# Optimization experiments

Hardware: AMD Instinct MI355X
Metric: run time of the kernel (lower is better)

Reference implementation:

```python
import jax, jax.numpy as jnp
import numpy as np

B, T, F, H, D, NC = 4096, 16, 64, 512, 15, 2  # batch, seq, feat(+time), hidden, mem window, classes
FX = F - 1  # real feature dim (channel 0 is the time delta)


def setup_inputs() -> dict:
    key = jax.random.key(0)
    ks = jax.random.split(key, 24)
    u = lambda k, shape, s=0.05: jax.random.uniform(k, shape, jnp.float32, -s, s)
    return {
        "inputs": jax.random.normal(ks[0], (B, T, F), jnp.float32),
        "init_proj": u(ks[1], (F, H)),            # self._init, keras random_uniform
        "hc_init": jnp.zeros((1, H), jnp.float32),  # h/c init (zeros initializer)
        # TH_cell: fused LSTM gates [i,f,o,c]
        "Wx": u(ks[2], (FX, 4 * H)),
        "Uh": u(ks[3], (H, 4 * H)),
        "Wt": u(ks[4], (1, 3 * H)),               # time delta -> i,f,o gates
        "b": jnp.zeros((4 * H,), jnp.float32),
        # time-aware gate
        "WxT": u(ks[5], (FX, H)),
        "WtT": u(ks[6], (1, H)),
        "bT": jnp.zeros((H,), jnp.float32),
        # historical attention over str_mem
        "Wa": u(ks[7], (H, H)),
        "Wb": u(ks[8], (H, H)),
        "va": u(ks[9], (H,)),
        "ba": jnp.zeros((H,), jnp.float32),
        # interaction / output combine
        "We": u(ks[10], (H, H)),
        "Wg": u(ks[11], (H, H)),
        "bh": jnp.zeros((H,), jnp.float32),
        # classifier head (Dropout is identity at inference)
        "W1": u(ks[12], (H, 256)),
        "b1": jnp.zeros((256,), jnp.float32),
        "W2": u(ks[13], (256, 32)),
        "b2": jnp.zeros((32,), jnp.float32),
        "W3": u(ks[14], (32, NC)),
        "b3": jnp.zeros((NC,), jnp.float32),
    }


def reference(inputs, init_proj, hc_init, Wx, Uh, Wt, b, WxT, WtT, bT,
              Wa, Wb, va, ba, We, Wg, bh, W1, b1, W2, b2, W3, b3):
    Bn = inputs.shape[0]
    # str_mem init: ones_like(inputs) @ _init, drop last step -> [B, T-1=D, H]
    str_mem = jnp.matmul(jnp.ones_like(inputs), init_proj)[:, :-1]
    h = jnp.broadcast_to(hc_init, (Bn, H))
    c = jnp.broadcast_to(hc_init, (Bn, H))
    x_seq = jnp.transpose(inputs[..., 1:], (1, 0, 2))   # [T, B, FX]
    t_seq = jnp.transpose(inputs[..., :1], (1, 0, 2))   # [T, B, 1]

    def step(carry, xt):
        h, c, mem = carry
        x, t = xt
        z = x @ Wx + h @ Uh + b                      # [B, 4H]
        zi, zf, zo, zc = jnp.split(z, 4, axis=-1)
        ti, tf_, to = jnp.split(t @ Wt, 3, axis=-1)
        i = jax.nn.sigmoid(zi + ti)
        f = jax.nn.sigmoid(zf + tf_)
        o = jax.nn.sigmoid(zo + to)
        chat = jnp.tanh(zc)
        Tg = jax.nn.sigmoid(x @ WxT + jax.nn.sigmoid(t @ WtT) + bT)  # time-aware gate
        c_new = f * c + i * chat + Tg * chat
        h_cur = o * jnp.tanh(c_new)
        # historical attention over sliding memory [B, D, H]
        e = jnp.einsum('bdh,h->bd',
                       jnp.tanh(jnp.einsum('bdh,hk->bdk', mem, Wa)
                                + (h_cur @ Wb + ba)[:, None, :]), va)
        alpha = jax.nn.softmax(e, axis=1)
        ctx = jnp.einsum('bd,bdh->bh', alpha, mem)
        h_new = jnp.tanh(ctx @ We + h_cur @ Wg + bh)
        mem_new = jnp.concatenate([mem[:, 1:], h_new[:, None]], axis=1)
        return (h_new, c_new, mem_new), None

    (h, c, str_mem), _ = jax.lax.scan(step, (h, c, str_mem), (x_seq, t_seq))
    hd = jax.nn.relu(h @ W1 + b1)
    hd = jax.nn.relu(hd @ W2 + b2)
    return jax.nn.softmax(hd @ W3 + b3, axis=-1)
```

## Files before the change

kernel.cpp:

```cpp
#include <hip/hip_runtime.h>
#include <hip/hip_bf16.h>

typedef __bf16 bf16;
typedef __attribute__((ext_vector_type(8))) __bf16 bf16x8;
typedef __attribute__((ext_vector_type(4))) float floatx4;

#define HDIM 512
#define BATCH 4096
#define TSTEPS 16
#define KA 576
#define NR 3584

typedef const __attribute__((address_space(1))) void gvoid;
typedef __attribute__((address_space(3))) void svoid;

__device__ __forceinline__ float ftanh(float x) {
  float xx = fminf(fmaxf(x, -15.f), 15.f);
  float t = __expf(2.f * xx);
  return (t - 1.f) / (t + 1.f);
}
__device__ __forceinline__ float fsigm(float x) { return 1.0f / (1.0f + __expf(-x)); }

__device__ __forceinline__ float waveAllSum(float v) {
#pragma unroll
  for (int off = 32; off > 0; off >>= 1) v += __shfl_xor(v, off, 64);
  return v;
}

__global__ __launch_bounds__(256, 4)
void gemm1_fused(const bf16* __restrict__ A1, const bf16* __restrict__ A2,
                 const bf16* __restrict__ BT,
                 const float* __restrict__ tdT, const float* __restrict__ bvec,
                 const float* __restrict__ WtT, const float* __restrict__ bT,
                 float* __restrict__ cbuf, bf16* __restrict__ hcur,
                 bf16* __restrict__ waSlot, bf16* __restrict__ weSlot) {
  constexpr int BM = 128, BN = 112, BK = 64;
  constexpr int TM = 2, TN = 7;
  __shared__ __align__(16) bf16 As[BM * BK];
  __shared__ __align__(16) bf16 Bs[BN * BK];

  const int tid = threadIdx.x;
  const int lane = tid & 63;
  const int wv = tid >> 6;
  const int quad = lane >> 4;
  const int lr = lane & 15;
  const int bid = blockIdx.x;
  const int xcd = bid & 7;
  const int p = bid >> 3;
  const int n_idx = (xcd << 2) | (p >> 5);
  const int m_idx = p & 31;
  const int m0 = m_idx * BM;
  const int n0 = n_idx * BN;
  const int g8 = lane >> 3;
  const int cl = (lane & 7) ^ g8;

  floatx4 acc[TM][TN];
#pragma unroll
  for (int i = 0; i < TM; ++i)
#pragma unroll
    for (int j = 0; j < TN; ++j) {
      acc[i][j][0] = 0.f; acc[i][j][1] = 0.f; acc[i][j][2] = 0.f; acc[i][j][3] = 0.f;
    }

  {
#pragma unroll
    for (int s = 0; s < 4; ++s) {
      const int g = wv * 4 + s;
      const int r = g * 8 + g8;
      const bf16* src = A1 + (size_t)(m0 + r) * 64 + cl * 8;
      __builtin_amdgcn_global_load_lds((gvoid*)src, (svoid*)&As[g * 512], 16, 0, 0);
    }
#pragma unroll
    for (int s = 0; s < 4; ++s) {
      const int g = wv * 4 + s;
      if (g < 10) {
        const int r = g * 8 + g8;
        const bf16* src = BT + (size_t)(n0 + r) * KA + cl * 8;
        __builtin_amdgcn_global_load_lds((gvoid*)src, (svoid*)&Bs[g * 512], 16, 0, 0);
      }
    }
    __syncthreads();
#pragma unroll
    for (int s = 0; s < 2; ++s) {
      const int lc = s * 4 + quad;
      bf16x8 afr[TM];
      bf16x8 bfr[5];
#pragma unroll
      for (int i = 0; i < TM; ++i) {
        const int r = wv * 32 + i * 16 + lr;
        afr[i] = *reinterpret_cast<const bf16x8*>(&As[r * 64 + ((lc ^ (r & 7)) << 3)]);
      }
#pragma unroll
      for (int j = 0; j < 5; ++j) {
        const int r = j * 16 + lr;
        bfr[j] = *reinterpret_cast<const bf16x8*>(&Bs[r * 64 + ((lc ^ (r & 7)) << 3)]);
      }
#pragma unroll
      for (int i = 0; i < TM; ++i)
#pragma unroll
        for (int j = 0; j < 5; ++j)
          acc[i][j] = __builtin_amdgcn_mfma_f32_16x16x32_bf16(afr[i], bfr[j], acc[i][j], 0, 0, 0);
    }
  }

  constexpr int JMAP[6] = {0, 1, 2, 3, 5, 6};
  for (int kt = 1; kt < KA / BK; ++kt) {
    const int kb = kt * BK;
    __syncthreads();
#pragma unroll
    for (int s = 0; s < 4; ++s) {
      const int g = wv * 4 + s;
      const int r = g * 8 + g8;
      const bf16* src = A2 + (size_t)(m0 + r) * 512 + (kb - 64) + cl * 8;
      __builtin_amdgcn_global_load_lds((gvoid*)src, (svoid*)&As[g * 512], 16, 0, 0);
    }
#pragma unroll
    for (int s = 0; s < 4; ++s) {
      const int g = wv * 4 + s;
      if (g < 14 && g != 8 && g != 9) {
        const int r = g * 8 + g8;
        const bf16* src = BT + (size_t)(n0 + r) * KA + kb + cl * 8;
        __builtin_amdgcn_global_load_lds((gvoid*)src, (svoid*)&Bs[g * 512], 16, 0, 0);
      }
    }
    __syncthreads();
#pragma unroll
    for (int s = 0; s < 2; ++s) {
      const int lc = s * 4 + quad;
      bf16x8 afr[TM];
      bf16x8 bfr[6];
#pragma unroll
      for (int i = 0; i < TM; ++i) {
        const int r = wv * 32 + i * 16 + lr;
        afr[i] = *reinterpret_cast<const bf16x8*>(&As[r * 64 + ((lc ^ (r & 7)) << 3)]);
      }
#pragma unroll
      for (int jj = 0; jj < 6; ++jj) {
        const int r = JMAP[jj] * 16 + lr;
        bfr[jj] = *reinterpret_cast<const bf16x8*>(&Bs[r * 64 + ((lc ^ (r & 7)) << 3)]);
      }
#pragma unroll
      for (int i = 0; i < TM; ++i)
#pragma unroll
        for (int jj = 0; jj < 6; ++jj)
          acc[i][JMAP[jj]] =
              __builtin_amdgcn_mfma_f32_16x16x32_bf16(afr[i], bfr[jj], acc[i][JMAP[jj]], 0, 0, 0);
    }
  }

  const int hcol = n_idx * 16 + lr;
  const float bvi = bvec[hcol], bvf = bvec[512 + hcol];
  const float bvo = bvec[1024 + hcol], bvc = bvec[1536 + hcol];
  const float wtt = WtT[hcol], bt_ = bT[hcol];
#pragma unroll
  for (int i = 0; i < TM; ++i) {
#pragma unroll
    for (int r = 0; r < 4; ++r) {
      const int m = m0 + wv * 32 + i * 16 + quad * 4 + r;
      const float td = tdT[m];
      const size_t o = (size_t)m * 512 + hcol;
      const float c_old = cbuf[o];
      const float i_ = fsigm(acc[i][0][r] + bvi);
      const float f_ = fsigm(acc[i][1][r] + bvf);
      const float o_ = fsigm(acc[i][2][r] + bvo);
      const float ch = ftanh(acc[i][3][r] + bvc);
      const float tg = fsigm(acc[i][4][r] + fsigm(td * wtt) + bt_);
      const float cn = f_ * c_old + (i_ + tg) * ch;
      cbuf[o] = cn;
      hcur[o] = (bf16)(o_ * ftanh(cn));
      waSlot[o] = (bf16)acc[i][5][r];
      weSlot[o] = (bf16)acc[i][6][r];
    }
  }
}

__global__ __launch_bounds__(256, 4)
void gemm2_kernel(const bf16* __restrict__ hcur, const bf16* __restrict__ wbwgT,
                  const float* __restrict__ baPad, bf16* __restrict__ hWbG) {
  __shared__ __align__(16) bf16 As[128 * 64];
  __shared__ __align__(16) bf16 Bs[64 * 64];

  const int tid = threadIdx.x;
  const int lane = tid & 63;
  const int wv = tid >> 6;
  const int quad = lane >> 4;
  const int lr = lane & 15;
  const int bid = blockIdx.x;
  const int m0 = (bid >> 4) * 128;
  const int n0 = (bid & 15) * 64;
  const int g8 = lane >> 3;
  const int cl = (lane & 7) ^ g8;

  floatx4 acc[2][4];
#pragma unroll
  for (int i = 0; i < 2; ++i)
#pragma unroll
    for (int j = 0; j < 4; ++j) {
      acc[i][j][0] = 0.f; acc[i][j][1] = 0.f; acc[i][j][2] = 0.f; acc[i][j][3] = 0.f;
    }

  for (int kt = 0; kt < 8; ++kt) {
    const int kb = kt * 64;
    __syncthreads();
#pragma unroll
    for (int s = 0; s < 4; ++s) {
      const int g = wv * 4 + s;
      const int r = g * 8 + g8;
      const bf16* src = hcur + (size_t)(m0 + r) * 512 + kb + cl * 8;
      __builtin_amdgcn_global_load_lds((gvoid*)src, (svoid*)&As[g * 512], 16, 0, 0);
    }
#pragma unroll
    for (int s = 0; s < 2; ++s) {
      const int g = wv * 2 + s;
      const int r = g * 8 + g8;
      const bf16* src = wbwgT + (size_t)(n0 + r) * 512 + kb + cl * 8;
      __builtin_amdgcn_global_load_lds((gvoid*)src, (svoid*)&Bs[g * 512], 16, 0, 0);
    }
    __syncthreads();
#pragma unroll
    for (int s = 0; s < 2; ++s) {
      const int lc = s * 4 + quad;
      bf16x8 afr[2];
      bf16x8 bfr[4];
#pragma unroll
      for (int i = 0; i < 2; ++i) {
        const int r = wv * 32 + i * 16 + lr;
        afr[i] = *reinterpret_cast<const bf16x8*>(&As[r * 64 + ((lc ^ (r & 7)) << 3)]);
      }
#pragma unroll
      for (int j = 0; j < 4; ++j) {
        const int r = j * 16 + lr;
        bfr[j] = *reinterpret_cast<const bf16x8*>(&Bs[r * 64 + ((lc ^ (r & 7)) << 3)]);
      }
#pragma unroll
      for (int i = 0; i < 2; ++i)
#pragma unroll
        for (int j = 0; j < 4; ++j)
          acc[i][j] = __builtin_amdgcn_mfma_f32_16x16x32_bf16(afr[i], bfr[j], acc[i][j], 0, 0, 0);
    }
  }

#pragma unroll
  for (int i = 0; i < 2; ++i) {
#pragma unroll
    for (int j = 0; j < 4; ++j) {
      const int n = n0 + j * 16 + lr;
      const float bb = baPad[n];
#pragma unroll
      for (int r = 0; r < 4; ++r) {
        const int m = m0 + wv * 32 + i * 16 + quad * 4 + r;
        hWbG[(size_t)m * 1024 + n] = (bf16)(acc[i][j][r] + bb);
      }
    }
  }
}

template <int BM, int BN>
__global__ __launch_bounds__(256)
void gemm_glds_kernel(const bf16* __restrict__ A1, int ld1, int K1,
                      const bf16* __restrict__ A2, int ld2,
                      const bf16* __restrict__ BT, int K, int mode,
                      float* __restrict__ outF, int ldF, const float* __restrict__ colBias,
                      bf16* __restrict__ outBa, int ldBa, const float* __restrict__ cBias2) {
  constexpr int BK = 32;
  constexpr int WM = BM / 2;
  constexpr int WN = BN / 2;
  constexpr int TM = WM / 16;
  constexpr int TN = WN / 16;
  constexpr int AIW = BM / 64;
  constexpr int BIW = BN / 64;
  __shared__ __align__(16) bf16 As[BM * BK];
  __shared__ __align__(16) bf16 Bs[BN * BK];

  const int tid = threadIdx.x;
  const int lane = tid & 63;
  const int wv = tid >> 6;
  const int wy = wv >> 1;
  const int wx = wv & 1;
  const int quad = lane >> 4;
  const int lr = lane & 15;
  const int m0 = blockIdx.y * BM;
  const int n0 = blockIdx.x * BN;
  const int sw = quad ^ ((lr >> 1) & 3);
  const int srow = lane >> 2;
  const int cl = (lane & 3) ^ ((lane >> 3) & 3);

  floatx4 acc[TM][TN];
#pragma unroll
  for (int i = 0; i < TM; ++i)
#pragma unroll
    for (int j = 0; j < TN; ++j) {
      acc[i][j][0] = 0.f; acc[i][j][1] = 0.f; acc[i][j][2] = 0.f; acc[i][j][3] = 0.f;
    }

  const int kTiles = K / BK;
  for (int kt = 0; kt < kTiles; ++kt) {
    const int kb = kt * BK;
    __syncthreads();
#pragma unroll
    for (int s = 0; s < AIW; ++s) {
      const int rbase = (wv * AIW + s) * 16;
      const int r = rbase + srow;
      const int col = kb + cl * 8;
      const bf16* src = (col < K1) ? (A1 + (size_t)(m0 + r) * ld1 + col)
                                   : (A2 + (size_t)(m0 + r) * ld2 + (col - K1));
      __builtin_amdgcn_global_load_lds((gvoid*)src, (svoid*)&As[rbase * BK], 16, 0, 0);
    }
#pragma unroll
    for (int s = 0; s < BIW; ++s) {
      const int rbase = (wv * BIW + s) * 16;
      const int r = rbase + srow;
      const bf16* src = BT + (size_t)(n0 + r) * K + kb + cl * 8;
      __builtin_amdgcn_global_load_lds((gvoid*)src, (svoid*)&Bs[rbase * BK], 16, 0, 0);
    }
    __syncthreads();
    bf16x8 afr[TM];
    bf16x8 bfr[TN];
#pragma unroll
    for (int i = 0; i < TM; ++i)
      afr[i] = *reinterpret_cast<const bf16x8*>(&As[(wy * WM + i * 16 + lr) * BK + sw * 8]);
#pragma unroll
    for (int j = 0; j < TN; ++j)
      bfr[j] = *reinterpret_cast<const bf16x8*>(&Bs[(wx * WN + j * 16 + lr) * BK + sw * 8]);
#pragma unroll
    for (int i = 0; i < TM; ++i)
#pragma unroll
      for (int j = 0; j < TN; ++j)
        acc[i][j] = __builtin_amdgcn_mfma_f32_16x16x32_bf16(afr[i], bfr[j], acc[i][j], 0, 0, 0);
  }

#pragma unroll
  for (int i = 0; i < TM; ++i) {
#pragma unroll
    for (int j = 0; j < TN; ++j) {
#pragma unroll
      for (int r = 0; r < 4; ++r) {
        int m = m0 + wy * WM + i * 16 + quad * 4 + r;
        int n = n0 + wx * WN + j * 16 + lr;
        float v = acc[i][j][r];
        if (mode == 0) {
          if (colBias != nullptr) v += colBias[n];
          outF[(size_t)m * ldF + n] = v;
        } else {
          v += cBias2[n];
          v = v > 0.f ? v : 0.f;
          outBa[(size_t)m * ldBa + n] = (bf16)v;
        }
      }
    }
  }
}

__global__ void pack_wcombT_kernel(const float* __restrict__ Wx, const float* __restrict__ Uh,
                                   const float* __restrict__ Wt, const float* __restrict__ WxT,
                                   const float* __restrict__ Wa, const float* __restrict__ We,
                                   bf16* __restrict__ out) {
  int idx = blockIdx.x * 256 + threadIdx.x;
  if (idx >= NR * KA) return;
  int n = idx / KA;
  int k = idx - n * KA;
  int blk = n / 112;
  int rem = n - blk * 112;
  int role = rem >> 4;
  int h = blk * 16 + (rem & 15);
  float v = 0.f;
  if (k < 63) {
    if (role < 4) v = Wx[k * 2048 + role * 512 + h];
    else if (role == 4) v = WxT[k * 512 + h];
  } else if (k == 63) {
    if (role < 3) v = Wt[role * 512 + h];
  } else {
    int kh = k - 64;
    if (role < 4) v = Uh[kh * 2048 + role * 512 + h];
    else if (role == 5) v = Wa[kh * 512 + h];
    else if (role == 6) v = We[kh * 512 + h];
  }
  out[idx] = (bf16)v;
}

__global__ void pack_t_kernel(const float* __restrict__ in, bf16* __restrict__ out, int N, int K) {
  int idx = blockIdx.x * 256 + threadIdx.x;
  if (idx >= N * K) return;
  int n = idx / K;
  int j = idx - n * K;
  out[idx] = (bf16)in[(size_t)j * N + n];
}

__global__ __launch_bounds__(512)
void setup_misc_kernel(const float* __restrict__ init_proj, const float* __restrict__ Wa,
                       const float* __restrict__ We, const float* __restrict__ ba,
                       float* __restrict__ sWa, float* __restrict__ sWe,
                       float* __restrict__ baPad) {
  __shared__ float s_sh[HDIM];
  int h = threadIdx.x;
  float acc = 0.f;
  for (int f = 0; f < 64; ++f) acc += init_proj[f * HDIM + h];
  s_sh[h] = acc;
  baPad[h] = ba[h];
  baPad[HDIM + h] = 0.f;
  __syncthreads();
  float a2 = 0.f, a3 = 0.f;
  for (int i = 0; i < HDIM; ++i) {
    a2 += s_sh[i] * Wa[i * HDIM + h];
    a3 += s_sh[i] * We[i * HDIM + h];
  }
  sWa[h] = a2;
  sWe[h] = a3;
}

__global__ void zero_state_kernel(float* __restrict__ c, bf16* __restrict__ h) {
  int idx = blockIdx.x * 256 + threadIdx.x;
  if (idx >= BATCH * HDIM) return;
  c[idx] = 0.f;
  h[idx] = (bf16)0.f;
}

__global__ void build_x_kernel(const float* __restrict__ inputs, bf16* __restrict__ xbuf,
                               float* __restrict__ tdT) {
  int idx = blockIdx.x * 256 + threadIdx.x;
  if (idx >= TSTEPS * BATCH * 64) return;
  int c = idx & 63;
  int bt = idx >> 6;
  int t = bt >> 12;
  int b = bt & 4095;
  float v;
  if (c < 63) {
    v = inputs[(size_t)b * 1024 + t * 64 + 1 + c];
  } else {
    v = inputs[(size_t)b * 1024 + t * 64];
    tdT[t * BATCH + b] = v;
  }
  xbuf[idx] = (bf16)v;
}

template <int K>
__global__ __launch_bounds__(256, 4)
void attention_kernel(const bf16* __restrict__ hWbG,
                      const float* __restrict__ sWa, const float* __restrict__ sWe,
                      const float* __restrict__ va, const float* __restrict__ bh,
                      const bf16* __restrict__ histWa, const bf16* __restrict__ histWe,
                      bf16* __restrict__ hbuf) {
  constexpr float C = 2.8853900817779268f;
  constexpr float L2E = 1.4426950408889634f;
  constexpr int CH = 4;
  constexpr int NC = (K + CH - 1) / CH;
  const int b = blockIdx.x * 4 + (threadIdx.x >> 6);
  const int lane = threadIdx.x & 63;
  const bf16* wbp = hWbG + (size_t)b * 1024 + lane * 8;
  bf16x8 wbv = *reinterpret_cast<const bf16x8*>(wbp);
  bf16x8 wgv = *reinterpret_cast<const bf16x8*>(wbp + 512);

  const bf16* pa = histWa + (size_t)b * HDIM + lane * 8;
  const bf16* pe = histWe + (size_t)b * HDIM + lane * 8;
  constexpr size_t RSTR = (size_t)BATCH * HDIM;

  bf16x8 buf[2][CH];
  if (NC > 0) {
#pragma unroll
    for (int r = 0; r < CH; ++r)
      if (r < K) buf[0][r] = *reinterpret_cast<const bf16x8*>(pa + (size_t)r * RSTR);
    asm volatile("" ::: "memory");
  }

  float wb2[8], vv[8];
  float svv = 0.f;
#pragma unroll
  for (int i = 0; i < 8; ++i) {
    wb2[i] = (float)wbv[i] * C;
    vv[i] = va[lane * 8 + i];
    svv += vv[i];
  }

  float e_init = 0.f;
  if (K < 15) {
    float p = 0.f;
#pragma unroll
    for (int i = 0; i < 8; ++i) {
      float r = __builtin_amdgcn_rcpf(exp2f(fmaf(sWa[lane * 8 + i], C, wb2[i])) + 1.f);
      p = fmaf(vv[i], r, p);
    }
    e_init = waveAllSum(fmaf(-2.f, p, svv));
  }

  float q[K > 0 ? K : 1];
#pragma unroll
  for (int c = 0; c < NC; ++c) {
    if (c + 1 < NC) {
#pragma unroll
      for (int r = 0; r < CH; ++r) {
        const int j = (c + 1) * CH + r;
        if (j < K)
          buf[(c + 1) & 1][r] = *reinterpret_cast<const bf16x8*>(pa + (size_t)j * RSTR);
      }
      asm volatile("" ::: "memory");
    }
#pragma unroll
    for (int r = 0; r < CH; ++r) {
      const int j = c * CH + r;
      if (j < K) {
        float p = 0.f;
#pragma unroll
        for (int i = 0; i < 8; ++i) {
          float t = __builtin_amdgcn_rcpf(
              exp2f(fmaf((float)buf[c & 1][r][i], C, wb2[i])) + 1.f);
          p = fmaf(vv[i], t, p);
        }
        q[j] = fmaf(-2.f, p, svv);
      }
    }
  }

  bf16x8 ebuf[2][CH];
  if (NC > 0) {
#pragma unroll
    for (int r = 0; r < CH; ++r)
      if (r < K) ebuf[0][r] = *reinterpret_cast<const bf16x8*>(pe + (size_t)r * RSTR);
    asm volatile("" ::: "memory");
  }

#pragma unroll
  for (int off = 32; off > 0; off >>= 1) {
#pragma unroll
    for (int j = 0; j < K; ++j) q[j] += __shfl_xor(q[j], off, 64);
  }

  float mx = (K < 15) ? e_init : -1e30f;
#pragma unroll
  for (int j = 0; j < K; ++j) mx = fmaxf(mx, q[j]);
  float winit = (K < 15) ? (float)(15 - K) * exp2f((e_init - mx) * L2E) : 0.f;
  float denom = winit;
  float w[K > 0 ? K : 1];
#pragma unroll
  for (int j = 0; j < K; ++j) {
    w[j] = exp2f((q[j] - mx) * L2E);
    denom += w[j];
  }
  const float inv = __builtin_amdgcn_rcpf(denom);

  float cx[8];
  const float ai = winit * inv;
#pragma unroll
  for (int i = 0; i < 8; ++i) cx[i] = ai * sWe[lane * 8 + i];
#pragma unroll
  for (int c = 0; c < NC; ++c) {
    if (c + 1 < NC) {
#pragma unroll
      for (int r = 0; r < CH; ++r) {
        const int j = (c + 1) * CH + r;
        if (j < K)
          ebuf[(c + 1) & 1][r] = *reinterpret_cast<const bf16x8*>(pe + (size_t)j * RSTR);
      }
      asm volatile("" ::: "memory");
    }
#pragma unroll
    for (int r = 0; r < CH; ++r) {
      const int j = c * CH + r;
      if (j < K) {
        const float aj = w[j] * inv;
#pragma unroll
        for (int i = 0; i < 8; ++i) cx[i] = fmaf(aj, (float)ebuf[c & 1][r][i], cx[i]);
      }
    }
  }

  bf16x8 hnew;
#pragma unroll
  for (int i = 0; i < 8; ++i) {
    float s = cx[i] + (float)wgv[i] + bh[lane * 8 + i];
    float r = __builtin_amdgcn_rcpf(exp2f(s * C) + 1.f);
    hnew[i] = (bf16)fmaf(-2.f, r, 1.f);
  }
  *reinterpret_cast<bf16x8*>(hbuf + (size_t)b * HDIM + lane * 8) = hnew;
}

__global__ __launch_bounds__(256)
void head_kernel(const bf16* __restrict__ hd1, const float* __restrict__ W2,
                 const float* __restrict__ b2, const float* __restrict__ W3,
                 const float* __restrict__ b3, float* __restrict__ out) {
  __shared__ float W2s[256 * 32];
  __shared__ float b2s[32];
  __shared__ float W3s[64];
  __shared__ float b3s[2];
  for (int i = threadIdx.x; i < 256 * 32; i += 256) W2s[i] = W2[i];
  if (threadIdx.x < 32) b2s[threadIdx.x] = b2[threadIdx.x];
  if (threadIdx.x < 64) W3s[threadIdx.x] = W3[threadIdx.x];
  if (threadIdx.x < 2) b3s[threadIdx.x] = b3[threadIdx.x];
  __syncthreads();
  int row = blockIdx.x * 256 + threadIdx.x;
  float acc[32];
#pragma unroll
  for (int j = 0; j < 32; ++j) acc[j] = b2s[j];
  const bf16* hp = hd1 + (size_t)row * 256;
  for (int i = 0; i < 256; ++i) {
    float hv = (float)hp[i];
#pragma unroll
    for (int j = 0; j < 32; ++j) acc[j] += hv * W2s[i * 32 + j];
  }
  float l0 = b3s[0], l1 = b3s[1];
#pragma unroll
  for (int j = 0; j < 32; ++j) {
    float r = fmaxf(acc[j], 0.f);
    l0 += r * W3s[j * 2];
    l1 += r * W3s[j * 2 + 1];
  }
  float m = fmaxf(l0, l1);
  float e0 = __expf(l0 - m), e1 = __expf(l1 - m);
  float inv = 1.f / (e0 + e1);
  out[(size_t)row * 2] = e0 * inv;
  out[(size_t)row * 2 + 1] = e1 * inv;
}

extern "C" void kernel_launch(void* const* d_in, const int* in_sizes, int n_in,
                              void* d_out, int out_size, void* d_ws, size_t ws_size,
                              hipStream_t stream) {
  const float* inputs    = (const float*)d_in[0];
  const float* init_proj = (const float*)d_in[1];
  const float* Wx  = (const float*)d_in[3];
  const float* Uh  = (const float*)d_in[4];
  const float* Wt  = (const float*)d_in[5];
  const float* bv  = (const float*)d_in[6];
  const float* WxT = (const float*)d_in[7];
  const float* WtT = (const float*)d_in[8];
  const float* bT  = (const float*)d_in[9];
  const float* Wa  = (const float*)d_in[10];
  const float* Wb  = (const float*)d_in[11];
  const float* va  = (const float*)d_in[12];
  const float* ba  = (const float*)d_in[13];
  const float* We  = (const float*)d_in[14];
  const float* Wg  = (const float*)d_in[15];
  const float* bh  = (const float*)d_in[16];
  const float* W1  = (const float*)d_in[17];
  const float* b1  = (const float*)d_in[18];
  const float* W2  = (const float*)d_in[19];
  const float* b2  = (const float*)d_in[20];
  const float* W3  = (const float*)d_in[21];
  const float* b3  = (const float*)d_in[22];
  float* out = (float*)d_out;

  char* wp = (char*)d_ws;
  auto carve = [&](size_t bytes) -> void* {
    void* p = (void*)wp;
    wp += (bytes + 255) & ~(size_t)255;
    return p;
  };
  bf16* wcombT = (bf16*)carve((size_t)NR * KA * 2);
  bf16* wbwgT  = (bf16*)carve((size_t)1024 * 512 * 2);
  bf16* w1T    = (bf16*)carve((size_t)256 * 512 * 2);
  float* sWa   = (float*)carve(512 * 4);
  float* sWe   = (float*)carve(512 * 4);
  float* baPad = (float*)carve(1024 * 4);
  bf16* xbuf   = (bf16*)carve((size_t)TSTEPS * BATCH * 64 * 2);
  float* tdT   = (float*)carve((size_t)TSTEPS * BATCH * 4);
  float* cbuf  = (float*)carve((size_t)BATCH * HDIM * 4);
  bf16* hbuf   = (bf16*)carve((size_t)BATCH * HDIM * 2);
  bf16* hcur   = (bf16*)carve((size_t)BATCH * HDIM * 2);
  bf16* hWbG   = (bf16*)carve((size_t)BATCH * 1024 * 2);
  bf16* histWa = (bf16*)carve((size_t)16 * BATCH * HDIM * 2);
  bf16* histWe = (bf16*)carve((size_t)16 * BATCH * HDIM * 2);
  bf16* hd1    = (bf16*)carve((size_t)BATCH * 256 * 2);

  build_x_kernel<<<(TSTEPS * BATCH * 64) / 256, 256, 0, stream>>>(inputs, xbuf, tdT);
  pack_wcombT_kernel<<<(NR * KA + 255) / 256, 256, 0, stream>>>(Wx, Uh, Wt, WxT, Wa, We, wcombT);
  pack_t_kernel<<<(512 * 512) / 256, 256, 0, stream>>>(Wb, wbwgT, 512, 512);
  pack_t_kernel<<<(512 * 512) / 256, 256, 0, stream>>>(Wg, wbwgT + (size_t)512 * 512, 512, 512);
  pack_t_kernel<<<(256 * 512) / 256, 256, 0, stream>>>(W1, w1T, 256, 512);
  setup_misc_kernel<<<1, 512, 0, stream>>>(init_proj, Wa, We, ba, sWa, sWe, baPad);
  zero_state_kernel<<<(BATCH * HDIM) / 256, 256, 0, stream>>>(cbuf, hbuf);

#define ATTN_LAUNCH(KK)                                                              \
  case KK:                                                                           \
    attention_kernel<KK><<<BATCH / 4, 256, 0, stream>>>(hWbG, sWa, sWe, va, bh,      \
                                                        histWa, histWe, hbuf);       \
    break;

  for (int t = 0; t < TSTEPS; ++t) {
    bf16* waSlot = histWa + (size_t)((t + 15) & 15) * BATCH * HDIM;
    bf16* weSlot = histWe + (size_t)((t + 15) & 15) * BATCH * HDIM;
    gemm1_fused<<<1024, 256, 0, stream>>>(
        xbuf + (size_t)t * BATCH * 64, hbuf, wcombT, tdT + (size_t)t * BATCH, bv, WtT, bT,
        cbuf, hcur, waSlot, weSlot);
    gemm2_kernel<<<512, 256, 0, stream>>>(hcur, wbwgT, baPad, hWbG);
    switch (t) {
      ATTN_LAUNCH(0) ATTN_LAUNCH(1) ATTN_LAUNCH(2) ATTN_LAUNCH(3)
      ATTN_LAUNCH(4) ATTN_LAUNCH(5) ATTN_LAUNCH(6) ATTN_LAUNCH(7)
      ATTN_LAUNCH(8) ATTN_LAUNCH(9) ATTN_LAUNCH(10) ATTN_LAUNCH(11)
      ATTN_LAUNCH(12) ATTN_LAUNCH(13) ATTN_LAUNCH(14) ATTN_LAUNCH(15)
    }
  }
#undef ATTN_LAUNCH

  gemm_glds_kernel<64, 128><<<dim3(256 / 128, BATCH / 64), 256, 0, stream>>>(
      hbuf, 512, 512, hbuf, 512, w1T, 512, 3, nullptr, 0, nullptr, hd1, 256, b1);
  head_kernel<<<BATCH / 256, 256, 0, stream>>>(hd1, W2, b2, W3, b3, out);
}
```

Measured before the change: 997.5 us.

## Fuse attention softmax and context into one online-softmax pass; faster gate activations

The attention kernel now loads the Wa- and We-projected history rows together and computes scores, softmax and context in a single streaming pass with an online-softmax rescale. This replaces the earlier two separate passes over memory, where all scores were held in registers and reduced at the end. Separately, the LSTM gate epilogue swaps expf/divide sigmoid and tanh for exp2f plus a hardware reciprocal. In exchange there are extra exp2f rescale operations per memory slot and more registers held for the double-buffered loads. Per-chunk wave reductions also sit on the critical path.

```diff
diff --git a/kernel.cpp b/kernel.cpp
--- a/kernel.cpp
+++ b/kernel.cpp
@@ -20,6 +20,13 @@
   return (t - 1.f) / (t + 1.f);
 }
 __device__ __forceinline__ float fsigm(float x) { return 1.0f / (1.0f + __expf(-x)); }
+
+__device__ __forceinline__ float ftanh2(float x) {
+  return fmaf(-2.f, __builtin_amdgcn_rcpf(exp2f(x * 2.8853900817779268f) + 1.f), 1.f);
+}
+__device__ __forceinline__ float fsigm2(float x) {
+  return __builtin_amdgcn_rcpf(1.f + exp2f(-x * 1.4426950408889634f));
+}
 
 __device__ __forceinline__ float waveAllSum(float v) {
 #pragma unroll
@@ -160,14 +167,14 @@
       const float td = tdT[m];
       const size_t o = (size_t)m * 512 + hcol;
       const float c_old = cbuf[o];
-      const float i_ = fsigm(acc[i][0][r] + bvi);
-      const float f_ = fsigm(acc[i][1][r] + bvf);
-      const float o_ = fsigm(acc[i][2][r] + bvo);
-      const float ch = ftanh(acc[i][3][r] + bvc);
-      const float tg = fsigm(acc[i][4][r] + fsigm(td * wtt) + bt_);
+      const float i_ = fsigm2(acc[i][0][r] + bvi);
+      const float f_ = fsigm2(acc[i][1][r] + bvf);
+      const float o_ = fsigm2(acc[i][2][r] + bvo);
+      const float ch = ftanh2(acc[i][3][r] + bvc);
+      const float tg = fsigm2(acc[i][4][r] + fsigm2(td * wtt) + bt_);
       const float cn = f_ * c_old + (i_ + tg) * ch;
       cbuf[o] = cn;
-      hcur[o] = (bf16)(o_ * ftanh(cn));
+      hcur[o] = (bf16)(o_ * ftanh2(cn));
       waSlot[o] = (bf16)acc[i][5][r];
       weSlot[o] = (bf16)acc[i][6][r];
     }
@@ -454,11 +461,14 @@
   const bf16* pe = histWe + (size_t)b * HDIM + lane * 8;
   constexpr size_t RSTR = (size_t)BATCH * HDIM;
 
-  bf16x8 buf[2][CH];
+  bf16x8 abuf[2][CH], ebuf[2][CH];
   if (NC > 0) {
 #pragma unroll
     for (int r = 0; r < CH; ++r)
-      if (r < K) buf[0][r] = *reinterpret_cast<const bf16x8*>(pa + (size_t)r * RSTR);
+      if (r < K) {
+        abuf[0][r] = *reinterpret_cast<const bf16x8*>(pa + (size_t)r * RSTR);
+        ebuf[0][r] = *reinterpret_cast<const bf16x8*>(pe + (size_t)r * RSTR);
+      }
     asm volatile("" ::: "memory");
   }
 
@@ -471,7 +481,7 @@
     svv += vv[i];
   }
 
-  float e_init = 0.f;
+  float m, d, u[8];
   if (K < 15) {
     float p = 0.f;
 #pragma unroll
@@ -479,21 +489,31 @@
       float r = __builtin_amdgcn_rcpf(exp2f(fmaf(sWa[lane * 8 + i], C, wb2[i])) + 1.f);
       p = fmaf(vv[i], r, p);
     }
-    e_init = waveAllSum(fmaf(-2.f, p, svv));
-  }
-
-  float q[K > 0 ? K : 1];
+    m = waveAllSum(fmaf(-2.f, p, svv));
+    d = (float)(15 - K);
+#pragma unroll
+    for (int i = 0; i < 8; ++i) u[i] = d * sWe[lane * 8 + i];
+  } else {
+    m = -3.0e38f;
+    d = 0.f;
+#pragma unroll
+    for (int i = 0; i < 8; ++i) u[i] = 0.f;
+  }
+
 #pragma unroll
   for (int c = 0; c < NC; ++c) {
     if (c + 1 < NC) {
 #pragma unroll
       for (int r = 0; r < CH; ++r) {
         const int j = (c + 1) * CH + r;
-        if (j < K)
-          buf[(c + 1) & 1][r] = *reinterpret_cast<const bf16x8*>(pa + (size_t)j * RSTR);
+        if (j < K) {
+          abuf[(c + 1) & 1][r] = *reinterpret_cast<const bf16x8*>(pa + (size_t)j * RSTR);
+          ebuf[(c + 1) & 1][r] = *reinterpret_cast<const bf16x8*>(pe + (size_t)j * RSTR);
+        }
       }
       asm volatile("" ::: "memory");
     }
+    float q[CH];
 #pragma unroll
     for (int r = 0; r < CH; ++r) {
       const int j = c * CH + r;
@@ -502,71 +522,39 @@
 #pragma unroll
         for (int i = 0; i < 8; ++i) {
           float t = __builtin_amdgcn_rcpf(
-              exp2f(fmaf((float)buf[c & 1][r][i], C, wb2[i])) + 1.f);
+              exp2f(fmaf((float)abuf[c & 1][r][i], C, wb2[i])) + 1.f);
           p = fmaf(vv[i], t, p);
         }
-        q[j] = fmaf(-2.f, p, svv);
-      }
-    }
-  }
-
-  bf16x8 ebuf[2][CH];
-  if (NC > 0) {
-#pragma unroll
-    for (int r = 0; r < CH; ++r)
-      if (r < K) ebuf[0][r] = *reinterpret_cast<const bf16x8*>(pe + (size_t)r * RSTR);
-    asm volatile("" ::: "memory");
-  }
-
-#pragma unroll
-  for (int off = 32; off > 0; off >>= 1) {
-#pragma unroll
-    for (int j = 0; j < K; ++j) q[j] += __shfl_xor(q[j], off, 64);
-  }
-
-  float mx = (K < 15) ? e_init : -1e30f;
-#pragma unroll
-  for (int j = 0; j < K; ++j) mx = fmaxf(mx, q[j]);
-  float winit = (K < 15) ? (float)(15 - K) * exp2f((e_init - mx) * L2E) : 0.f;
-  float denom = winit;
-  float w[K > 0 ? K : 1];
-#pragma unroll
-  for (int j = 0; j < K; ++j) {
-    w[j] = exp2f((q[j] - mx) * L2E);
-    denom += w[j];
-  }
-  const float inv = __builtin_amdgcn_rcpf(denom);
-
-  float cx[8];
-  const float ai = winit * inv;
-#pragma unroll
-  for (int i = 0; i < 8; ++i) cx[i] = ai * sWe[lane * 8 + i];
-#pragma unroll
-  for (int c = 0; c < NC; ++c) {
-    if (c + 1 < NC) {
-#pragma unroll
-      for (int r = 0; r < CH; ++r) {
-        const int j = (c + 1) * CH + r;
-        if (j < K)
-          ebuf[(c + 1) & 1][r] = *reinterpret_cast<const bf16x8*>(pe + (size_t)j * RSTR);
-      }
-      asm volatile("" ::: "memory");
+        q[r] = fmaf(-2.f, p, svv);
+      }
+    }
+#pragma unroll
+    for (int off = 32; off > 0; off >>= 1) {
+#pragma unroll
+      for (int r = 0; r < CH; ++r)
+        if (c * CH + r < K) q[r] += __shfl_xor(q[r], off, 64);
     }
 #pragma unroll
     for (int r = 0; r < CH; ++r) {
       const int j = c * CH + r;
       if (j < K) {
-        const float aj = w[j] * inv;
-#pragma unroll
-        for (int i = 0; i < 8; ++i) cx[i] = fmaf(aj, (float)ebuf[c & 1][r][i], cx[i]);
-      }
-    }
-  }
-
+        const float nm = fmaxf(m, q[r]);
+        const float sc = exp2f((m - nm) * L2E);
+        const float w = exp2f((q[r] - nm) * L2E);
+        d = fmaf(d, sc, w);
+#pragma unroll
+        for (int i = 0; i < 8; ++i)
+          u[i] = fmaf(u[i], sc, w * (float)ebuf[c & 1][r][i]);
+        m = nm;
+      }
+    }
+  }
+
+  const float inv = __builtin_amdgcn_rcpf(d);
   bf16x8 hnew;
 #pragma unroll
   for (int i = 0; i < 8; ++i) {
-    float s = cx[i] + (float)wgv[i] + bh[lane * 8 + i];
+    float s = fmaf(u[i], inv, (float)wgv[i] + bh[lane * 8 + i]);
     float r = __builtin_amdgcn_rcpf(exp2f(s * C) + 1.f);
     hnew[i] = (bf16)fmaf(-2.f, r, 1.f);
   }
```

Measured after the change: 1.023 ms. 1.03x slower.
